# Optimization experiments

Hardware: AMD Instinct MI355X
Metric: run time of the kernel (lower is better)

## Reference

```python
import jax, jax.numpy as jnp
import numpy as np

HIDDEN = 1024
ARC = 500
BATCH = 16
SEQ = 512


def setup_inputs() -> dict:
    key = jax.random.key(0)
    ks = jax.random.split(key, 12)
    s_h = 1.0 / np.sqrt(HIDDEN)
    s_a = 1.0 / np.sqrt(ARC)
    return {
        "hidden_states": jax.random.normal(ks[0], (BATCH, SEQ, HIDDEN), dtype=jnp.float32),
        # head MLP: Linear(hidden->arc), ReLU, (Dropout eval=identity), Linear(arc->arc)
        "w1h": jax.random.uniform(ks[1], (ARC, HIDDEN), jnp.float32, -s_h, s_h),
        "b1h": jax.random.uniform(ks[2], (ARC,), jnp.float32, -s_h, s_h),
        "w2h": jax.random.uniform(ks[3], (ARC, ARC), jnp.float32, -s_a, s_a),
        "b2h": jax.random.uniform(ks[4], (ARC,), jnp.float32, -s_a, s_a),
        # dep MLP
        "w1d": jax.random.uniform(ks[5], (ARC, HIDDEN), jnp.float32, -s_h, s_h),
        "b1d": jax.random.uniform(ks[6], (ARC,), jnp.float32, -s_h, s_h),
        "w2d": jax.random.uniform(ks[7], (ARC, ARC), jnp.float32, -s_a, s_a),
        "b2d": jax.random.uniform(ks[8], (ARC,), jnp.float32, -s_a, s_a),
        # nn.Bilinear(arc, arc, 1, bias=True): weight [1, arc, arc], bias [1]
        "Wb": jax.random.uniform(ks[9], (ARC, ARC), jnp.float32, -s_a, s_a),
        "bb": jax.random.uniform(ks[10], (1,), jnp.float32, -s_a, s_a),
    }


def reference(hidden_states, w1h, b1h, w2h, b2h, w1d, b1d, w2d, b2d, Wb, bb):
    # MLPs (dropout is identity at inference)
    head = jnp.maximum(hidden_states @ w1h.T + b1h, 0.0) @ w2h.T + b2h  # [B,S,A]
    dep = jnp.maximum(hidden_states @ w1d.T + b1d, 0.0) @ w2d.T + b2d  # [B,S,A]
    # seq_len <= 512 already; chunked bilinear == two GEMMs:
    # scores[b,i,j] = head[b,i] @ Wb @ dep[b,j] + bb
    headW = head @ Wb  # [B,S,A]
    arc_scores = jnp.einsum("bia,bja->bij", headW, dep) + bb[0]  # [B,S,S]
    return arc_scores
```

## Files before the change

### kernel.cpp

```cpp
#include <hip/hip_runtime.h>
#include <hip/hip_bf16.h>


#define HIDDEN 1024
#define ARC 500
#define AP 512
#define ROWS 8192

typedef __attribute__((ext_vector_type(4))) float f32x4;
typedef __attribute__((ext_vector_type(8))) short short8;

static __device__ __forceinline__ ushort f2bf(float f) {
  union { float f; unsigned u; } v; v.f = f;
  unsigned r = v.u + 0x7fffu + ((v.u >> 16) & 1u);
  return (ushort)(r >> 16);
}

__global__ void k_conv_hs(const float4* __restrict__ in, ushort* __restrict__ out, int n4) {
  int i = blockIdx.x * blockDim.x + threadIdx.x;
  int st = gridDim.x * blockDim.x;
  for (; i < n4; i += st) {
    float4 v = in[i];
    ushort4 o;
    o.x = f2bf(v.x); o.y = f2bf(v.y); o.z = f2bf(v.z); o.w = f2bf(v.w);
    *(ushort4*)(out + (size_t)i * 4) = o;
  }
}

__global__ void k_prep(const float* __restrict__ w1h, const float* __restrict__ b1h,
                       const float* __restrict__ w1d, const float* __restrict__ b1d,
                       const float* __restrict__ w2h, const float* __restrict__ b2h,
                       const float* __restrict__ w2d, const float* __restrict__ b2d,
                       const float* __restrict__ Wb,
                       ushort* __restrict__ W1, ushort* __restrict__ WbT,
                       ushort* __restrict__ w2hT, ushort* __restrict__ W2,
                       float* __restrict__ b1c) {
  const int bid = blockIdx.x;
  const int tid = threadIdx.x;
  if (bid < 4096) {
    int idx = bid * 256 + tid;
    int n = idx >> 10, k = idx & 1023;
    float v = 0.f;
    if (n < ARC) v = w1h[(size_t)n * HIDDEN + k];
    else if (n >= AP && n < AP + ARC) v = w1d[(size_t)(n - AP) * HIDDEN + k];
    W1[idx] = f2bf(v);
  } else if (bid < 5120) {
    int idx = (bid - 4096) * 256 + tid;
    int a = idx >> 9, j = idx & 511;
    float v = (a < ARC && j < ARC) ? Wb[(size_t)j * ARC + a] : 0.f;
    WbT[idx] = f2bf(v);
  } else if (bid < 6144) {
    int idx = (bid - 5120) * 256 + tid;
    int k = idx >> 9, j = idx & 511;
    float v = 0.f;
    if (j < ARC) {
      if (k < ARC) v = w2h[(size_t)j * ARC + k];
      else if (k == 511) v = b2h[j];
    }
    w2hT[idx] = f2bf(v);
  } else if (bid < 7168) {
    int idx = (bid - 6144) * 256 + tid;
    int n = idx >> 9, k = idx & 511;
    float v = 0.f;
    if (n < ARC) {
      if (k < ARC) v = w2d[(size_t)n * ARC + k];
      else if (k == 511) v = b2d[n];
    }
    W2[idx] = f2bf(v);
  } else {
    int i = (bid - 7168) * 256 + tid;
    float v = 0.f;
    if (i < ARC) v = b1h[i];
    else if (i == 511 || i == 1023) v = 1.f;
    else if (i >= AP && i < AP + ARC) v = b1d[i - AP];
    b1c[i] = v;
  }
}

template <bool RELU, bool OUT_BF16, int BIAS_MODE, int BN>
__global__ __launch_bounds__(256)
void k_gemm_bt(const ushort* __restrict__ A, const ushort* __restrict__ B,
               const float* __restrict__ bias, void* __restrict__ Cv,
               int lda, int ldb, int ldc, int K,
               long aBS, long bBS, long cBS) {
  constexpr int WC = BN / 2;
  constexpr int NFR = WC / 16;
  __shared__ ushort As[128 * 32];
  __shared__ ushort Bs[BN * 32];

  const int gx = gridDim.x, gy = gridDim.y;
  const int gxy = gx * gy;
  const int nwg = gxy * gridDim.z;
  const int flat = (blockIdx.z * gy + blockIdx.y) * gx + blockIdx.x;
  const int q = nwg >> 3;
  const int f2 = (flat & 7) * q + (flat >> 3);
  const int bz = f2 / gxy;
  const int rm = f2 - bz * gxy;
  const int by = rm / gx;
  const int bx = rm - by * gx;

  const int t = threadIdx.x;
  const int w = t >> 6;
  const int l = t & 63;
  A += (size_t)aBS * bz;
  B += (size_t)bBS * bz;
  const int tm = by * 128;
  const int tn = bx * BN;
  const int wr = w >> 1, wc = w & 1;

  f32x4 acc[4][NFR];
#pragma unroll
  for (int m = 0; m < 4; ++m)
#pragma unroll
    for (int n = 0; n < NFR; ++n) acc[m][n] = f32x4{0.f, 0.f, 0.f, 0.f};

  const int srow = w * 16 + (l >> 2);
  const int scol = (l & 3) * 8;
  const ushort* ag = A + (size_t)(tm + srow) * lda + scol;
  const ushort* bg = B + (size_t)(tn + srow) * ldb + scol;
  ushort* lA = As + w * 512;
  ushort* lB = Bs + w * 512;

  const int fr = l & 15, fh = l >> 4;
  const ushort* fA = As + (size_t)(wr * 64 + fr) * 32 + fh * 8;
  const ushort* fB = Bs + (size_t)(wc * WC + fr) * 32 + fh * 8;

  for (int kt = 0; kt < K; kt += 32) {
#pragma unroll
    for (int c = 0; c < 2; ++c)
      __builtin_amdgcn_global_load_lds(
          (const __attribute__((address_space(1))) void*)(ag + (size_t)c * 64 * lda + kt),
          (__attribute__((address_space(3))) void*)(lA + c * 2048), 16, 0, 0);
#pragma unroll
    for (int c = 0; c < BN / 64; ++c)
      __builtin_amdgcn_global_load_lds(
          (const __attribute__((address_space(1))) void*)(bg + (size_t)c * 64 * ldb + kt),
          (__attribute__((address_space(3))) void*)(lB + c * 2048), 16, 0, 0);
    asm volatile("s_waitcnt vmcnt(0)" ::: "memory");
    __syncthreads();

    short8 af[4], bf[NFR];
#pragma unroll
    for (int m = 0; m < 4; ++m) af[m] = *(const short8*)(fA + m * 16 * 32);
#pragma unroll
    for (int n = 0; n < NFR; ++n) bf[n] = *(const short8*)(fB + n * 16 * 32);
#pragma unroll
    for (int m = 0; m < 4; ++m)
#pragma unroll
      for (int n = 0; n < NFR; ++n)
        acc[m][n] = __builtin_amdgcn_mfma_f32_16x16x32_bf16(af[m], bf[n], acc[m][n], 0, 0, 0);
    __syncthreads();
  }

  const int cr = fh * 4;
  const float bscal = (BIAS_MODE == 2) ? bias[0] : 0.f;
#pragma unroll
  for (int m = 0; m < 4; ++m) {
#pragma unroll
    for (int n = 0; n < NFR; ++n) {
      const int col = tn + wc * WC + n * 16 + fr;
      const float bv = (BIAS_MODE == 1) ? bias[col] : bscal;
#pragma unroll
      for (int j = 0; j < 4; ++j) {
        const int row = tm + wr * 64 + m * 16 + cr + j;
        float v = acc[m][n][j] + bv;
        if (RELU) v = fmaxf(v, 0.f);
        if (OUT_BF16)
          ((ushort*)Cv)[(size_t)cBS * bz + (size_t)row * ldc + col] = f2bf(v);
        else
          ((float*)Cv)[(size_t)cBS * bz + (size_t)row * ldc + col] = v;
      }
    }
  }
}

extern "C" void kernel_launch(void* const* d_in, const int* in_sizes, int n_in,
                              void* d_out, int out_size, void* d_ws, size_t ws_size,
                              hipStream_t stream) {
  const float* hs  = (const float*)d_in[0];
  const float* w1h = (const float*)d_in[1];
  const float* b1h = (const float*)d_in[2];
  const float* w2h = (const float*)d_in[3];
  const float* b2h = (const float*)d_in[4];
  const float* w1d = (const float*)d_in[5];
  const float* b1d = (const float*)d_in[6];
  const float* w2d = (const float*)d_in[7];
  const float* b2d = (const float*)d_in[8];
  const float* Wb  = (const float*)d_in[9];
  const float* bb  = (const float*)d_in[10];

  char* ws = (char*)d_ws;
  ushort* hs_bf = (ushort*)(ws + 0);
  ushort* W1    = (ushort*)(ws + 16777216);
  ushort* WbT   = (ushort*)(ws + 18874368);
  ushort* w2hT  = (ushort*)(ws + 19398656);
  ushort* MT    = (ushort*)(ws + 19922944);
  ushort* W2    = (ushort*)(ws + 20447232);
  ushort* t1    = (ushort*)(ws + 20971520);
  ushort* hw    = (ushort*)(ws + 37748736);
  float*  b1c   = (float*)(ws + 54525952);
  float*  out   = (float*)d_out;

  k_conv_hs<<<2048, 256, 0, stream>>>((const float4*)hs, hs_bf, ROWS * HIDDEN / 4);
  k_prep<<<7172, 256, 0, stream>>>(w1h, b1h, w1d, b1d, w2h, b2h, w2d, b2d, Wb,
                                   W1, WbT, w2hT, W2, b1c);

  k_gemm_bt<false, true, 0, 128><<<dim3(4, 4, 1), 256, 0, stream>>>(
      WbT, w2hT, nullptr, MT, AP, AP, AP, AP, 0, 0, 0);

  k_gemm_bt<true, true, 1, 128><<<dim3(8, 64, 1), 256, 0, stream>>>(
      hs_bf, W1, b1c, t1, HIDDEN, HIDDEN, 1024, HIDDEN, 0, 0, 0);

  k_gemm_bt<false, true, 0, 128><<<dim3(4, 64, 2), 256, 0, stream>>>(
      t1, MT, nullptr, hw, 1024, AP, AP, AP,
      AP, (long)AP * AP, (long)ROWS * AP);

  k_gemm_bt<false, false, 2, 64><<<dim3(8, 4, 16), 256, 0, stream>>>(
      hw, hw + (size_t)ROWS * AP, bb, out, AP, AP, 512, AP,
      (long)512 * AP, (long)512 * AP, (long)512 * 512);
}
```

Baseline: 177.3 us.

## Double-buffer GEMM LDS tiles and merge prep and small GEMM launches

```diff
diff --git a/kernel.cpp b/kernel.cpp
--- a/kernel.cpp
+++ b/kernel.cpp
@@ -16,25 +16,14 @@
   return (ushort)(r >> 16);
 }
 
-__global__ void k_conv_hs(const float4* __restrict__ in, ushort* __restrict__ out, int n4) {
-  int i = blockIdx.x * blockDim.x + threadIdx.x;
-  int st = gridDim.x * blockDim.x;
-  for (; i < n4; i += st) {
-    float4 v = in[i];
-    ushort4 o;
-    o.x = f2bf(v.x); o.y = f2bf(v.y); o.z = f2bf(v.z); o.w = f2bf(v.w);
-    *(ushort4*)(out + (size_t)i * 4) = o;
-  }
-}
-
-__global__ void k_prep(const float* __restrict__ w1h, const float* __restrict__ b1h,
-                       const float* __restrict__ w1d, const float* __restrict__ b1d,
-                       const float* __restrict__ w2h, const float* __restrict__ b2h,
-                       const float* __restrict__ w2d, const float* __restrict__ b2d,
-                       const float* __restrict__ Wb,
-                       ushort* __restrict__ W1, ushort* __restrict__ WbT,
-                       ushort* __restrict__ w2hT, ushort* __restrict__ W2,
-                       float* __restrict__ b1c) {
+__global__ void k_prep_all(const float* __restrict__ w1h, const float* __restrict__ b1h,
+                           const float* __restrict__ w1d, const float* __restrict__ b1d,
+                           const float* __restrict__ w2h, const float* __restrict__ b2h,
+                           const float* __restrict__ w2d, const float* __restrict__ b2d,
+                           const float* __restrict__ Wb, const float4* __restrict__ hs,
+                           ushort* __restrict__ W1, ushort* __restrict__ WbT,
+                           ushort* __restrict__ w2hT, ushort* __restrict__ W2,
+                           float* __restrict__ b1c, ushort* __restrict__ hs_bf) {
   const int bid = blockIdx.x;
   const int tid = threadIdx.x;
   if (bid < 4096) {
@@ -67,27 +56,144 @@
       else if (k == 511) v = b2d[n];
     }
     W2[idx] = f2bf(v);
-  } else {
+  } else if (bid < 7172) {
     int i = (bid - 7168) * 256 + tid;
     float v = 0.f;
     if (i < ARC) v = b1h[i];
     else if (i == 511 || i == 1023) v = 1.f;
     else if (i >= AP && i < AP + ARC) v = b1d[i - AP];
     b1c[i] = v;
-  }
-}
-
-template <bool RELU, bool OUT_BF16, int BIAS_MODE, int BN>
+  } else {
+    const int n4 = ROWS * HIDDEN / 4;
+    int i = (bid - 7172) * 256 + tid;
+    for (; i < n4; i += 2048 * 256) {
+      float4 v = hs[i];
+      ushort4 o;
+      o.x = f2bf(v.x); o.y = f2bf(v.y); o.z = f2bf(v.z); o.w = f2bf(v.w);
+      *(ushort4*)(hs_bf + (size_t)i * 4) = o;
+    }
+  }
+}
+
+template <int BN>
+__device__ __forceinline__ void gemm_body(
+    const ushort* __restrict__ A, const ushort* __restrict__ B,
+    const float* __restrict__ bias, int bias_mode,
+    void* __restrict__ C, int out_bf16, int relu,
+    int lda, int ldb, int ldc, int K, int tm, int tn, ushort* lds) {
+  constexpr int WC = BN / 2;
+  constexpr int NFR = WC / 16;
+  ushort* As0 = lds;
+  ushort* As1 = lds + 4096;
+  ushort* Bs0 = lds + 8192;
+  ushort* Bs1 = lds + 8192 + BN * 32;
+
+  const int t = threadIdx.x;
+  const int w = t >> 6;
+  const int l = t & 63;
+  const int wr = w >> 1, wc = w & 1;
+
+  f32x4 acc[4][NFR];
+#pragma unroll
+  for (int m = 0; m < 4; ++m)
+#pragma unroll
+    for (int n = 0; n < NFR; ++n) acc[m][n] = f32x4{0.f, 0.f, 0.f, 0.f};
+
+  const int srow = w * 16 + (l >> 2);
+  const int scol = (l & 3) * 8;
+  const ushort* ag = A + (size_t)(tm + srow) * lda + scol;
+  const ushort* bg = B + (size_t)(tn + srow) * ldb + scol;
+  const int lofs = w * 512;
+
+  const int fr = l & 15, fh = l >> 4;
+  const int fAo = (wr * 64 + fr) * 32 + fh * 8;
+  const int fBo = (wc * WC + fr) * 32 + fh * 8;
+
+  auto stage = [&](int kt, ushort* lA, ushort* lB) {
+#pragma unroll
+    for (int c = 0; c < 2; ++c)
+      __builtin_amdgcn_global_load_lds(
+          (const __attribute__((address_space(1))) void*)(ag + (size_t)c * 64 * lda + kt),
+          (__attribute__((address_space(3))) void*)(lA + lofs + c * 2048), 16, 0, 0);
+#pragma unroll
+    for (int c = 0; c < BN / 64; ++c)
+      __builtin_amdgcn_global_load_lds(
+          (const __attribute__((address_space(1))) void*)(bg + (size_t)c * 64 * ldb + kt),
+          (__attribute__((address_space(3))) void*)(lB + lofs + c * 2048), 16, 0, 0);
+  };
+  auto compute = [&](const ushort* As, const ushort* Bs) {
+    short8 af[4], bf[NFR];
+#pragma unroll
+    for (int m = 0; m < 4; ++m) af[m] = *(const short8*)(As + fAo + m * 16 * 32);
+#pragma unroll
+    for (int n = 0; n < NFR; ++n) bf[n] = *(const short8*)(Bs + fBo + n * 16 * 32);
+#pragma unroll
+    for (int m = 0; m < 4; ++m)
+#pragma unroll
+      for (int n = 0; n < NFR; ++n)
+        acc[m][n] = __builtin_amdgcn_mfma_f32_16x16x32_bf16(af[m], bf[n], acc[m][n], 0, 0, 0);
+  };
+
+  const int nt = K >> 5;
+  stage(0, As0, Bs0);
+  for (int ti = 0; ti < nt; ti += 2) {
+    __syncthreads();
+    if (ti + 1 < nt) stage((ti + 1) << 5, As1, Bs1);
+    compute(As0, Bs0);
+    __syncthreads();
+    if (ti + 2 < nt) stage((ti + 2) << 5, As0, Bs0);
+    compute(As1, Bs1);
+  }
+
+  const int cr = fh * 4;
+  const float bscal = (bias_mode == 2) ? bias[0] : 0.f;
+#pragma unroll
+  for (int m = 0; m < 4; ++m) {
+#pragma unroll
+    for (int n = 0; n < NFR; ++n) {
+      const int col = tn + wc * WC + n * 16 + fr;
+      const float bv = (bias_mode == 1) ? bias[col] : bscal;
+#pragma unroll
+      for (int j = 0; j < 4; ++j) {
+        const int row = tm + wr * 64 + m * 16 + cr + j;
+        float v = acc[m][n][j] + bv;
+        if (relu) v = fmaxf(v, 0.f);
+        if (out_bf16)
+          ((ushort*)C)[(size_t)row * ldc + col] = f2bf(v);
+        else
+          ((float*)C)[(size_t)row * ldc + col] = v;
+      }
+    }
+  }
+}
+
 __global__ __launch_bounds__(256)
-void k_gemm_bt(const ushort* __restrict__ A, const ushort* __restrict__ B,
-               const float* __restrict__ bias, void* __restrict__ Cv,
+void k_g1mt(const ushort* __restrict__ hs_bf, const ushort* __restrict__ W1,
+            const float* __restrict__ b1c, ushort* __restrict__ t1,
+            const ushort* __restrict__ WbT, const ushort* __restrict__ w2hT,
+            ushort* __restrict__ MTb) {
+  __shared__ ushort lds[16384];
+  const int flat = blockIdx.y * 8 + blockIdx.x;
+  const int f2 = (flat & 7) * 66 + (flat >> 3);
+  const int by = f2 >> 3, bx = f2 & 7;
+  if (by < 64) {
+    gemm_body<128>(hs_bf, W1, b1c, 1, t1, 1, 1,
+                   HIDDEN, HIDDEN, 1024, HIDDEN, by * 128, bx * 128, lds);
+  } else {
+    const int idx = (by - 64) * 8 + bx;
+    gemm_body<128>(WbT, w2hT, nullptr, 0, MTb, 1, 0,
+                   AP, AP, AP, AP, (idx >> 2) * 128, (idx & 3) * 128, lds);
+  }
+}
+
+template <int BN>
+__global__ __launch_bounds__(256)
+void k_gemm_rt(const ushort* __restrict__ A, const ushort* __restrict__ B,
+               const float* __restrict__ bias, int bias_mode,
+               void* __restrict__ C, int out_bf16, int relu,
                int lda, int ldb, int ldc, int K,
                long aBS, long bBS, long cBS) {
-  constexpr int WC = BN / 2;
-  constexpr int NFR = WC / 16;
-  __shared__ ushort As[128 * 32];
-  __shared__ ushort Bs[BN * 32];
-
+  __shared__ ushort lds[8192 + BN * 64];
   const int gx = gridDim.x, gy = gridDim.y;
   const int gxy = gx * gy;
   const int nwg = gxy * gridDim.z;
@@ -99,79 +205,12 @@
   const int by = rm / gx;
   const int bx = rm - by * gx;
 
-  const int t = threadIdx.x;
-  const int w = t >> 6;
-  const int l = t & 63;
-  A += (size_t)aBS * bz;
-  B += (size_t)bBS * bz;
-  const int tm = by * 128;
-  const int tn = bx * BN;
-  const int wr = w >> 1, wc = w & 1;
-
-  f32x4 acc[4][NFR];
-#pragma unroll
-  for (int m = 0; m < 4; ++m)
-#pragma unroll
-    for (int n = 0; n < NFR; ++n) acc[m][n] = f32x4{0.f, 0.f, 0.f, 0.f};
-
-  const int srow = w * 16 + (l >> 2);
-  const int scol = (l & 3) * 8;
-  const ushort* ag = A + (size_t)(tm + srow) * lda + scol;
-  const ushort* bg = B + (size_t)(tn + srow) * ldb + scol;
-  ushort* lA = As + w * 512;
-  ushort* lB = Bs + w * 512;
-
-  const int fr = l & 15, fh = l >> 4;
-  const ushort* fA = As + (size_t)(wr * 64 + fr) * 32 + fh * 8;
-  const ushort* fB = Bs + (size_t)(wc * WC + fr) * 32 + fh * 8;
-
-  for (int kt = 0; kt < K; kt += 32) {
-#pragma unroll
-    for (int c = 0; c < 2; ++c)
-      __builtin_amdgcn_global_load_lds(
-          (const __attribute__((address_space(1))) void*)(ag + (size_t)c * 64 * lda + kt),
-          (__attribute__((address_space(3))) void*)(lA + c * 2048), 16, 0, 0);
-#pragma unroll
-    for (int c = 0; c < BN / 64; ++c)
-      __builtin_amdgcn_global_load_lds(
-          (const __attribute__((address_space(1))) void*)(bg + (size_t)c * 64 * ldb + kt),
-          (__attribute__((address_space(3))) void*)(lB + c * 2048), 16, 0, 0);
-    asm volatile("s_waitcnt vmcnt(0)" ::: "memory");
-    __syncthreads();
-
-    short8 af[4], bf[NFR];
-#pragma unroll
-    for (int m = 0; m < 4; ++m) af[m] = *(const short8*)(fA + m * 16 * 32);
-#pragma unroll
-    for (int n = 0; n < NFR; ++n) bf[n] = *(const short8*)(fB + n * 16 * 32);
-#pragma unroll
-    for (int m = 0; m < 4; ++m)
-#pragma unroll
-      for (int n = 0; n < NFR; ++n)
-        acc[m][n] = __builtin_amdgcn_mfma_f32_16x16x32_bf16(af[m], bf[n], acc[m][n], 0, 0, 0);
-    __syncthreads();
-  }
-
-  const int cr = fh * 4;
-  const float bscal = (BIAS_MODE == 2) ? bias[0] : 0.f;
-#pragma unroll
-  for (int m = 0; m < 4; ++m) {
-#pragma unroll
-    for (int n = 0; n < NFR; ++n) {
-      const int col = tn + wc * WC + n * 16 + fr;
-      const float bv = (BIAS_MODE == 1) ? bias[col] : bscal;
-#pragma unroll
-      for (int j = 0; j < 4; ++j) {
-        const int row = tm + wr * 64 + m * 16 + cr + j;
-        float v = acc[m][n][j] + bv;
-        if (RELU) v = fmaxf(v, 0.f);
-        if (OUT_BF16)
-          ((ushort*)Cv)[(size_t)cBS * bz + (size_t)row * ldc + col] = f2bf(v);
-        else
-          ((float*)Cv)[(size_t)cBS * bz + (size_t)row * ldc + col] = v;
-      }
-    }
-  }
+  const ushort* Az = A + (size_t)aBS * bz;
+  const ushort* Bz = B + (size_t)bBS * bz;
+  void* Cz = out_bf16 ? (void*)((ushort*)C + (size_t)cBS * bz)
+                      : (void*)((float*)C + (size_t)cBS * bz);
+  gemm_body<BN>(Az, Bz, bias, bias_mode, Cz, out_bf16, relu,
+                lda, ldb, ldc, K, by * 128, bx * BN, lds);
 }
 
 extern "C" void kernel_launch(void* const* d_in, const int* in_sizes, int n_in,
@@ -201,21 +240,17 @@
   float*  b1c   = (float*)(ws + 54525952);
   float*  out   = (float*)d_out;
 
-  k_conv_hs<<<2048, 256, 0, stream>>>((const float4*)hs, hs_bf, ROWS * HIDDEN / 4);
-  k_prep<<<7172, 256, 0, stream>>>(w1h, b1h, w1d, b1d, w2h, b2h, w2d, b2d, Wb,
-                                   W1, WbT, w2hT, W2, b1c);
-
-  k_gemm_bt<false, true, 0, 128><<<dim3(4, 4, 1), 256, 0, stream>>>(
-      WbT, w2hT, nullptr, MT, AP, AP, AP, AP, 0, 0, 0);
-
-  k_gemm_bt<true, true, 1, 128><<<dim3(8, 64, 1), 256, 0, stream>>>(
-      hs_bf, W1, b1c, t1, HIDDEN, HIDDEN, 1024, HIDDEN, 0, 0, 0);
-
-  k_gemm_bt<false, true, 0, 128><<<dim3(4, 64, 2), 256, 0, stream>>>(
-      t1, MT, nullptr, hw, 1024, AP, AP, AP,
+  k_prep_all<<<9220, 256, 0, stream>>>(w1h, b1h, w1d, b1d, w2h, b2h, w2d, b2d,
+                                       Wb, (const float4*)hs,
+                                       W1, WbT, w2hT, W2, b1c, hs_bf);
+
+  k_g1mt<<<dim3(8, 66), 256, 0, stream>>>(hs_bf, W1, b1c, t1, WbT, w2hT, MT);
+
+  k_gemm_rt<128><<<dim3(4, 64, 2), 256, 0, stream>>>(
+      t1, MT, nullptr, 0, hw, 1, 0, 1024, AP, AP, AP,
       AP, (long)AP * AP, (long)ROWS * AP);
 
-  k_gemm_bt<false, false, 2, 64><<<dim3(8, 4, 16), 256, 0, stream>>>(
-      hw, hw + (size_t)ROWS * AP, bb, out, AP, AP, 512, AP,
+  k_gemm_rt<64><<<dim3(8, 4, 16), 256, 0, stream>>>(
+      hw, hw + (size_t)ROWS * AP, bb, 2, out, 0, 0, AP, AP, 512, AP,
       (long)512 * AP, (long)512 * AP, (long)512 * 512);
 }
```

Result: faster. 173.1 us (-2.4%).
